# Performance work log

Hardware: AMD Instinct MI355X
Metric: run time of the kernel (lower is better)

The kernel has to match this reference:

```python
import jax, jax.numpy as jnp
import numpy as np

B, F, H = 128, 12288, 2048   # batch, flattened-image dim (3x64x64), MLP hidden
TAU = 0.1                    # constraint(x) = relu(x@W1)@w2 - TAU  (so constraint(0) = -TAU < 0)
THRESHOLD = 1e-3
MAX_STEPS = 30


def setup_inputs() -> dict:
    key = jax.random.key(0)
    k1, k2, k3 = jax.random.split(key, 3)
    x0 = jnp.zeros((B, F), jnp.float32)                 # anchor point, constraint(x0) < 0 by construction
    x = jax.random.normal(k1, (B, F), jnp.float32)
    W1 = jax.random.normal(k2, (F, H), jnp.float32) / np.float32(np.sqrt(F))
    w2 = jax.random.normal(k3, (H,), jnp.float32) / np.float32(np.sqrt(H))
    return {"x0": x0, "x": x, "W1": W1, "w2": w2}


def reference(x0, x, W1, w2):
    def fvals(c):  # per-sample constraint value at interpolation coeff c: [B]
        xc = (1.0 - c)[:, None] * x0 + c[:, None] * x
        return jax.nn.relu(xc @ W1) @ w2 - TAU

    # f(0) = -TAU < 0 (asserted in original). Check f(1): samples already feasible skip search.
    f1 = fvals(jnp.ones((B,), jnp.float32))
    inside = f1 <= 0.0

    a = jnp.zeros((B,), jnp.float32)
    b = jnp.ones((B,), jnp.float32)
    c = jnp.ones((B,), jnp.float32)
    done = inside  # feasible samples keep c = 1 (projected == x)

    def step(carry, _):
        a, b, c, done = carry
        cm = (a + b) * 0.5
        v = fvals(cm)
        upd = ~done
        hit = upd & (v >= -THRESHOLD) & (v < 0.0)   # -threshold <= f(c) < 0 -> converged
        go_a = upd & (v < 0.0) & ~hit               # same sign as f(a): move a
        go_b = upd & (v >= 0.0)                     # opposite sign: move b
        a = jnp.where(go_a, cm, a)
        b = jnp.where(go_b, cm, b)
        c = jnp.where(upd, cm, c)                   # freeze c once done
        done = done | hit
        return (a, b, c, done), None

    (a, b, c, done), _ = jax.lax.scan(step, (a, b, c, done), None, length=MAX_STEPS)

    c = jnp.where(inside, 1.0, c)
    proj = (1.0 - c)[:, None] * x0 + c[:, None] * x
    # Original raises ConvergenceError -> NaN fill for non-converged samples.
    return jnp.where(done[:, None], proj, jnp.float32(jnp.nan))
```

## Files before the change

kernel.cpp:

```cpp
#include <hip/hip_runtime.h>
#include <hip/hip_bf16.h>

#define BB 128
#define FF 12288
#define HH 2048
#define TAU_F 0.1f
#define THR_F 1e-3f
#define NKG (FF / 8)
#define BH (BB * HH)
#define NFLAGS 192
#define SKD 16

typedef __attribute__((ext_vector_type(4))) float f32x4;
typedef __attribute__((ext_vector_type(8))) short s16x8;
typedef __attribute__((ext_vector_type(8))) unsigned short u16x8;

__device__ __forceinline__ void barrier_lds() {
    asm volatile("s_waitcnt lgkmcnt(0)\ns_barrier" ::: "memory");
}

__device__ __forceinline__ void bsplit(float v, unsigned short& h, unsigned short& l) {
    unsigned int u  = __float_as_uint(v);
    unsigned int rh = (u + 0x7fffu + ((u >> 16) & 1u)) >> 16;
    float hf = __uint_as_float(rh << 16);
    float lf = v - hf;
    unsigned int ul = __float_as_uint(lf);
    unsigned int rl = (ul + 0x7fffu + ((ul >> 16) & 1u)) >> 16;
    h = (unsigned short)rh;
    l = (unsigned short)rl;
}

__device__ __forceinline__ bool read_nz(const int* __restrict__ flags) {
    const int lane = threadIdx.x & 63;
    int v = 0;
    if (lane < NFLAGS / 4) {
        const int4 q = ((const int4*)flags)[lane];
        v = q.x | q.y | q.z | q.w;
    }
    return __any(v != 0);
}

__device__ __forceinline__ void presplit_blk(
    const float* __restrict__ X, unsigned short* __restrict__ AH,
    unsigned short* __restrict__ AL, int i, int t) {
    const int kg = i * 8 + (t & 7);
#pragma unroll
    for (int r = 0; r < 4; ++r) {
        const int m = (t >> 3) + r * 32;
        const float* src = X + (size_t)m * FF + kg * 8;
        u16x8 hv, lv;
#pragma unroll
        for (int j = 0; j < 8; ++j) {
            unsigned short h, lo;
            bsplit(src[j], h, lo);
            hv[j] = h; lv[j] = lo;
        }
        const size_t o = ((size_t)kg * BB + m) * 8;
        *(u16x8*)(AH + o) = hv;
        *(u16x8*)(AL + o) = lv;
    }
}

__global__ __launch_bounds__(256) void presplit_kernel(
    const float* __restrict__ x, const float* __restrict__ x0,
    unsigned short* __restrict__ Ah, unsigned short* __restrict__ Al,
    int* __restrict__ flags) {
    const int z = blockIdx.y;
    const int i = blockIdx.x;
    const int t = threadIdx.x;
    if (z == 0) {
        presplit_blk(x, Ah, Al, i, t);
        return;
    }
    __shared__ int snz[4];
    const int w = t >> 6, lane = t & 63;
    const int kg = i * 8 + (t & 7);
    int tnz = 0;
#pragma unroll
    for (int r = 0; r < 4; ++r) {
        const int m = (t >> 3) + r * 32;
        const float4* src = (const float4*)(x0 + (size_t)m * FF + kg * 8);
        const float4 a = src[0], b = src[1];
        tnz |= (a.x != 0.f) | (a.y != 0.f) | (a.z != 0.f) | (a.w != 0.f)
             | (b.x != 0.f) | (b.y != 0.f) | (b.z != 0.f) | (b.w != 0.f);
    }
    const int wnz = __any(tnz != 0) ? 1 : 0;
    if (lane == 0) snz[w] = wnz;
    __syncthreads();
    const int bnz = snz[0] | snz[1] | snz[2] | snz[3];
    if (t == 0) flags[i] = bnz;
    if (bnz) {
        const size_t zoff = (size_t)NKG * BB * 8;
        presplit_blk(x0, Ah + zoff, Al + zoff, i, t);
    }
}

__global__ __launch_bounds__(256, 2) void mfma_gemm_kernel(
    const unsigned short* __restrict__ Ah, const unsigned short* __restrict__ Al,
    const float* __restrict__ W1, float* __restrict__ P,
    const int* __restrict__ flags, int SK, int KC, int NIT) {
    const int z = blockIdx.y;
    if (z == 1 && !read_nz(flags)) return;

    const int nwg = gridDim.x;
    const int bx  = blockIdx.x;
    const int wg  = (bx & 7) * (nwg >> 3) + (bx >> 3);
    const int ct  = wg & 31;
    const int kc  = wg >> 5;

    const int t   = threadIdx.x;
    const int w   = t >> 6;
    const int l   = t & 63;
    const int kgl = l >> 4;
    const int li  = l & 15;

    __shared__ unsigned short lds[2][4096];

    const size_t zoffA = (size_t)z * NKG * BB * 8;
    const unsigned short* APH = Ah + zoffA;
    const unsigned short* APL = Al + zoffA;
    const bool zchk = (z == 1);

    f32x4 acc[2][4];
#pragma unroll
    for (int mt = 0; mt < 2; ++mt)
#pragma unroll
        for (int nt = 0; nt < 4; ++nt) acc[mt][nt] = (f32x4)0.f;

    const int kbase = kc * KC;
    const int kg0   = kbase >> 3;
    const int bkg = t >> 6;
    const int bn  = t & 63;

    s16x8 ahE[2], alE[2], ahO[2], alO[2];
    auto loadA = [&](s16x8* ah, s16x8* al, int it) {
        const int kg = kg0 + it * 4 + kgl;
        if (zchk && flags[kg >> 3] == 0) {
#pragma unroll
            for (int mt = 0; mt < 2; ++mt) { ah[mt] = (s16x8)0; al[mt] = (s16x8)0; }
            return;
        }
#pragma unroll
        for (int mt = 0; mt < 2; ++mt) {
            const size_t o = ((size_t)kg * BB + w * 32 + mt * 16 + li) * 8;
            ah[mt] = *(const s16x8*)(APH + o);
            al[mt] = *(const s16x8*)(APL + o);
        }
    };

    auto stageB_load = [&](int it, float* v) {
        const float* src = W1 + (size_t)(kbase + it * 32 + bkg * 8) * HH + ct * 64 + bn;
#pragma unroll
        for (int j = 0; j < 8; ++j) v[j] = src[(size_t)j * HH];
    };
    auto stageB_write = [&](int buf, const float* v) {
        u16x8 hv, lv;
#pragma unroll
        for (int j = 0; j < 8; ++j) {
            unsigned short h, lo;
            bsplit(v[j], h, lo);
            hv[j] = h; lv[j] = lo;
        }
        unsigned short* d = &lds[buf][(bkg * 64 + bn) * 8];
        *(u16x8*)(d)        = hv;
        *(u16x8*)(d + 2048) = lv;
    };
    auto computeR = [&](const s16x8* ah, const s16x8* al, int buf) {
        const unsigned short* L = lds[buf];
#pragma unroll
        for (int nt = 0; nt < 4; ++nt) {
            const int no = (kgl * 64 + nt * 16 + li) * 8;
            const s16x8 fbh = *(const s16x8*)&L[no];
            const s16x8 fbl = *(const s16x8*)&L[2048 + no];
#pragma unroll
            for (int mt = 0; mt < 2; ++mt) {
                acc[mt][nt] = __builtin_amdgcn_mfma_f32_16x16x32_bf16(ah[mt], fbh, acc[mt][nt], 0, 0, 0);
                acc[mt][nt] = __builtin_amdgcn_mfma_f32_16x16x32_bf16(ah[mt], fbl, acc[mt][nt], 0, 0, 0);
                acc[mt][nt] = __builtin_amdgcn_mfma_f32_16x16x32_bf16(al[mt], fbh, acc[mt][nt], 0, 0, 0);
            }
        }
    };

    float bv0[8], bv1[8], bv2[8], bv3[8];
    loadA(ahE, alE, 0);
    stageB_load(0, bv0);
    stageB_write(0, bv0);
    stageB_load(1, bv1);
    stageB_load(2, bv2);
    stageB_load(3, bv3);
    barrier_lds();

#define GPHASE(p, bvCur, bvNext, aCurH, aCurL, aNxtH, aNxtL)                  \
    {                                                                         \
        if (it + 4 + (p) < NIT) stageB_load(it + 4 + (p), bvCur);             \
        if (it + (p) + 1 < NIT) loadA(aNxtH, aNxtL, it + (p) + 1);            \
        computeR(aCurH, aCurL, (p) & 1);                                      \
        if (it + (p) + 1 < NIT) stageB_write(((p) + 1) & 1, bvNext);          \
        barrier_lds();                                                        \
    }

    for (int it = 0; it < NIT; it += 4) {
        GPHASE(0, bv0, bv1, ahE, alE, ahO, alO)
        GPHASE(1, bv1, bv2, ahO, alO, ahE, alE)
        GPHASE(2, bv2, bv3, ahE, alE, ahO, alO)
        GPHASE(3, bv3, bv0, ahO, alO, ahE, alE)
    }
#undef GPHASE

    float* dst = P + (size_t)(z * SK + kc) * BH;
    const int r0 = w * 32 + (l >> 4) * 4;
    const int c0 = ct * 64 + li;
#pragma unroll
    for (int mt = 0; mt < 2; ++mt)
#pragma unroll
        for (int nt = 0; nt < 4; ++nt)
#pragma unroll
            for (int r = 0; r < 4; ++r)
                dst[(size_t)(r0 + mt * 16 + r) * HH + c0 + nt * 16] = acc[mt][nt][r];
}

__device__ __forceinline__ void solve_linear(float S, float& c, bool& done) {
    const bool inside = (S - TAU_F <= 0.f);
    float a = 0.f, bh = 1.f;
    c = 1.f; done = inside;
    for (int it = 0; it < 30; ++it) {
        const float cm = 0.5f * (a + bh);
        const float v = cm * S - TAU_F;
        const bool upd  = !done;
        const bool hit  = upd && (v >= -THR_F) && (v < 0.f);
        const bool go_a = upd && (v < 0.f) && !hit;
        const bool go_b = upd && (v >= 0.f);
        a  = go_a ? cm : a;
        bh = go_b ? cm : bh;
        c  = upd  ? cm : c;
        done = done || hit;
    }
    c = inside ? 1.f : c;
}

__global__ __launch_bounds__(512) void bisect_write_kernel(
    const float* __restrict__ P, const float* __restrict__ w2,
    const float* __restrict__ x, const float* __restrict__ x0,
    const int* __restrict__ flags, float* __restrict__ out, int SK) {
    const int b    = blockIdx.x >> 1;
    const int half = blockIdx.x & 1;
    const int t = threadIdx.x;
    const int w = t >> 6;
    const int lane = t & 63;
    __shared__ float red[8];
    const bool nz = read_nz(flags);

    const f32x4* P1 = (const f32x4*)(P + (size_t)b * HH) + t;
    f32x4 u1 = (f32x4)0.f;
    for (int kc = 0; kc < SK; ++kc) {
        const f32x4 v = P1[(size_t)kc * (BH / 4)];
        u1.x += v.x; u1.y += v.y; u1.z += v.z; u1.w += v.w;
    }
    const f32x4 wv = ((const f32x4*)w2)[t];

    auto blockReduce = [&](float v) -> float {
#pragma unroll
        for (int off = 32; off > 0; off >>= 1) v += __shfl_xor(v, off);
        if (lane == 0) red[w] = v;
        __syncthreads();
        float s = 0.f;
#pragma unroll
        for (int i = 0; i < 8; ++i) s += red[i];
        __syncthreads();
        return s;
    };

    float c = 1.f;
    bool done = false;
    if (!nz) {
        float p = fmaxf(u1.x, 0.f) * wv.x;
        p = fmaf(fmaxf(u1.y, 0.f), wv.y, p);
        p = fmaf(fmaxf(u1.z, 0.f), wv.z, p);
        p = fmaf(fmaxf(u1.w, 0.f), wv.w, p);
        const float S = blockReduce(p);
        solve_linear(S, c, done);
    } else {
        const f32x4* P0 = (const f32x4*)(P + (size_t)(SK * BH) + (size_t)b * HH) + t;
        f32x4 u0 = (f32x4)0.f;
        for (int kc = 0; kc < SK; ++kc) {
            const f32x4 v = P0[(size_t)kc * (BH / 4)];
            u0.x += v.x; u0.y += v.y; u0.z += v.z; u0.w += v.w;
        }
        f32x4 dd;
        dd.x = u1.x - u0.x; dd.y = u1.y - u0.y;
        dd.z = u1.z - u0.z; dd.w = u1.w - u0.w;
        auto feval = [&](float cc) -> float {
            float p = fmaxf(fmaf(cc, dd.x, u0.x), 0.f) * wv.x;
            p = fmaf(fmaxf(fmaf(cc, dd.y, u0.y), 0.f), wv.y, p);
            p = fmaf(fmaxf(fmaf(cc, dd.z, u0.z), 0.f), wv.z, p);
            p = fmaf(fmaxf(fmaf(cc, dd.w, u0.w), 0.f), wv.w, p);
            return blockReduce(p) - TAU_F;
        };
        const float f1 = feval(1.f);
        const bool inside = (f1 <= 0.f);
        float a = 0.f, bh = 1.f;
        done = inside;
        for (int it = 0; it < 30; ++it) {
            const float cm = 0.5f * (a + bh);
            const float v = feval(cm);
            const bool upd  = !done;
            const bool hit  = upd && (v >= -THR_F) && (v < 0.f);
            const bool go_a = upd && (v < 0.f) && !hit;
            const bool go_b = upd && (v >= 0.f);
            a  = go_a ? cm : a;
            bh = go_b ? cm : bh;
            c  = upd  ? cm : c;
            done = done || hit;
        }
        c = inside ? 1.f : c;
    }

    const float nanv = __int_as_float(0x7fc00000);
    const int base = half * 1536;
    const float4* xr  = (const float4*)(x  + (size_t)b * FF) + base;
    const float4* x0r = (const float4*)(x0 + (size_t)b * FF) + base;
    float4* orow = (float4*)(out + (size_t)b * FF) + base;
    if (!done) {
        float4 o; o.x = o.y = o.z = o.w = nanv;
#pragma unroll
        for (int k2 = 0; k2 < 3; ++k2) orow[t + 512 * k2] = o;
    } else if (!nz) {
#pragma unroll
        for (int k2 = 0; k2 < 3; ++k2) {
            const int i = t + 512 * k2;
            float4 xv = xr[i], o;
            o.x = c * xv.x; o.y = c * xv.y; o.z = c * xv.z; o.w = c * xv.w;
            orow[i] = o;
        }
    } else {
#pragma unroll
        for (int k2 = 0; k2 < 3; ++k2) {
            const int i = t + 512 * k2;
            float4 xv = xr[i], zv = x0r[i], o;
            o.x = fmaf(c, xv.x - zv.x, zv.x);
            o.y = fmaf(c, xv.y - zv.y, zv.y);
            o.z = fmaf(c, xv.z - zv.z, zv.z);
            o.w = fmaf(c, xv.w - zv.w, zv.w);
            orow[i] = o;
        }
    }
}

__global__ __launch_bounds__(256) void zflags_kernel(
    const float4* __restrict__ x0, int* __restrict__ flags) {
    const int t = threadIdx.x;
    const int w = t >> 6, lane = t & 63;
    __shared__ int snz[4];
    int tnz = 0;
    const int base = blockIdx.x * 2048 + t;
#pragma unroll
    for (int j = 0; j < 8; ++j) {
        float4 v = x0[base + 256 * j];
        tnz |= (v.x != 0.f) | (v.y != 0.f) | (v.z != 0.f) | (v.w != 0.f);
    }
    const int wnz = __any(tnz != 0) ? 1 : 0;
    if (lane == 0) snz[w] = wnz;
    __syncthreads();
    if (t == 0) flags[blockIdx.x] = snz[0] | snz[1] | snz[2] | snz[3];
}

__global__ __launch_bounds__(256) void legacy_gemm_kernel(
    const float* __restrict__ x, const float* __restrict__ x0,
    const float* __restrict__ W1, float* __restrict__ P,
    const int* __restrict__ flags) {
    const int ct = blockIdx.x, z = blockIdx.z, t = threadIdx.x;
    if (z == 1 && !read_nz(flags)) return;
    const int cg = t & 7, rg = t >> 3;
    const int r0 = rg * 4, cc = ct * 64 + cg * 8;
    float acc[4][8];
#pragma unroll
    for (int i = 0; i < 4; ++i)
#pragma unroll
        for (int n = 0; n < 8; ++n) acc[i][n] = 0.f;
    const float* __restrict__ X = z ? x0 : x;
    for (int k = 0; k < FF; k += 4) {
        float xr[4][4];
#pragma unroll
        for (int i = 0; i < 4; ++i) {
            float4 v = *(const float4*)(X + (size_t)(r0 + i) * FF + k);
            xr[i][0] = v.x; xr[i][1] = v.y; xr[i][2] = v.z; xr[i][3] = v.w;
        }
        float wr[4][8];
#pragma unroll
        for (int j = 0; j < 4; ++j) {
            float4 a = *(const float4*)(W1 + (size_t)(k + j) * HH + cc);
            float4 b = *(const float4*)(W1 + (size_t)(k + j) * HH + cc + 4);
            wr[j][0] = a.x; wr[j][1] = a.y; wr[j][2] = a.z; wr[j][3] = a.w;
            wr[j][4] = b.x; wr[j][5] = b.y; wr[j][6] = b.z; wr[j][7] = b.w;
        }
#pragma unroll
        for (int j = 0; j < 4; ++j)
#pragma unroll
            for (int i = 0; i < 4; ++i)
#pragma unroll
                for (int n = 0; n < 8; ++n)
                    acc[i][n] = fmaf(xr[i][j], wr[j][n], acc[i][n]);
    }
    float* Pp = P + (size_t)z * BH;
#pragma unroll
    for (int i = 0; i < 4; ++i) {
        float4 o0, o1;
        o0.x = acc[i][0]; o0.y = acc[i][1]; o0.z = acc[i][2]; o0.w = acc[i][3];
        o1.x = acc[i][4]; o1.y = acc[i][5]; o1.z = acc[i][6]; o1.w = acc[i][7];
        *(float4*)(Pp + (size_t)(r0 + i) * HH + cc) = o0;
        *(float4*)(Pp + (size_t)(r0 + i) * HH + cc + 4) = o1;
    }
}

extern "C" void kernel_launch(void* const* d_in, const int* in_sizes, int n_in,
                              void* d_out, int out_size, void* d_ws, size_t ws_size,
                              hipStream_t stream) {
    const float* x0 = (const float*)d_in[0];
    const float* x  = (const float*)d_in[1];
    const float* W1 = (const float*)d_in[2];
    const float* w2 = (const float*)d_in[3];
    float* out = (float*)d_out;
    char* ws = (char*)d_ws;

    const size_t szA   = (size_t)2 * NKG * BB * 8 * sizeof(unsigned short);
    const size_t offAl = szA;
    const size_t offFl = 2 * szA;
    const size_t offP  = offFl + 1024;

    int SK = 0;
    const int cand[5] = {SKD, 8, 4, 2, 1};
    for (int i = 0; i < 5; ++i) {
        const size_t need = offP + (size_t)2 * cand[i] * BH * sizeof(float);
        if (ws_size >= need) { SK = cand[i]; break; }
    }

    if (SK > 0) {
        unsigned short* Ah = (unsigned short*)ws;
        unsigned short* Al = (unsigned short*)(ws + offAl);
        int*   flags = (int*)(ws + offFl);
        float* P     = (float*)(ws + offP);
        const int KC = FF / SK, NIT = KC / 32;

        presplit_kernel<<<dim3(NFLAGS, 2), 256, 0, stream>>>(x, x0, Ah, Al, flags);
        mfma_gemm_kernel<<<dim3(32 * SK, 2), 256, 0, stream>>>(Ah, Al, W1, P, flags, SK, KC, NIT);
        bisect_write_kernel<<<2 * BB, 512, 0, stream>>>(P, w2, x, x0, flags, out, SK);
    } else {
        float* P     = (float*)ws;
        int*   flags = (int*)(ws + (size_t)2 * BH * sizeof(float));
        zflags_kernel<<<NFLAGS, 256, 0, stream>>>((const float4*)x0, flags);
        legacy_gemm_kernel<<<dim3(32, 1, 2), 256, 0, stream>>>(x, x0, W1, P, flags);
        bisect_write_kernel<<<2 * BB, 512, 0, stream>>>(P, w2, x, x0, flags, out, 1);
    }
}
```

Measured before the change: 49.36 us.

## Double GEMM block to 512 threads with one M-tile per wave

```diff
diff --git a/kernel.cpp b/kernel.cpp
--- a/kernel.cpp
+++ b/kernel.cpp
@@ -14,6 +14,7 @@
 typedef __attribute__((ext_vector_type(4))) float f32x4;
 typedef __attribute__((ext_vector_type(8))) short s16x8;
 typedef __attribute__((ext_vector_type(8))) unsigned short u16x8;
+typedef __attribute__((ext_vector_type(4))) unsigned short u16x4;
 
 __device__ __forceinline__ void barrier_lds() {
     asm volatile("s_waitcnt lgkmcnt(0)\ns_barrier" ::: "memory");
@@ -95,7 +96,7 @@
     }
 }
 
-__global__ __launch_bounds__(256, 2) void mfma_gemm_kernel(
+__global__ __launch_bounds__(512, 4) void mfma_gemm_kernel(
     const unsigned short* __restrict__ Ah, const unsigned short* __restrict__ Al,
     const float* __restrict__ W1, float* __restrict__ P,
     const int* __restrict__ flags, int SK, int KC, int NIT) {
@@ -121,67 +122,56 @@
     const unsigned short* APL = Al + zoffA;
     const bool zchk = (z == 1);
 
-    f32x4 acc[2][4];
-#pragma unroll
-    for (int mt = 0; mt < 2; ++mt)
-#pragma unroll
-        for (int nt = 0; nt < 4; ++nt) acc[mt][nt] = (f32x4)0.f;
+    f32x4 acc[4];
+#pragma unroll
+    for (int nt = 0; nt < 4; ++nt) acc[nt] = (f32x4)0.f;
 
     const int kbase = kc * KC;
     const int kg0   = kbase >> 3;
-    const int bkg = t >> 6;
-    const int bn  = t & 63;
-
-    s16x8 ahE[2], alE[2], ahO[2], alO[2];
-    auto loadA = [&](s16x8* ah, s16x8* al, int it) {
+
+    s16x8 ahE, alE, ahO, alO;
+    auto loadA = [&](s16x8& ah, s16x8& al, int it) {
         const int kg = kg0 + it * 4 + kgl;
         if (zchk && flags[kg >> 3] == 0) {
-#pragma unroll
-            for (int mt = 0; mt < 2; ++mt) { ah[mt] = (s16x8)0; al[mt] = (s16x8)0; }
+            ah = (s16x8)0; al = (s16x8)0;
             return;
         }
-#pragma unroll
-        for (int mt = 0; mt < 2; ++mt) {
-            const size_t o = ((size_t)kg * BB + w * 32 + mt * 16 + li) * 8;
-            ah[mt] = *(const s16x8*)(APH + o);
-            al[mt] = *(const s16x8*)(APL + o);
-        }
+        const size_t o = ((size_t)kg * BB + w * 16 + li) * 8;
+        ah = *(const s16x8*)(APH + o);
+        al = *(const s16x8*)(APL + o);
     };
 
     auto stageB_load = [&](int it, float* v) {
-        const float* src = W1 + (size_t)(kbase + it * 32 + bkg * 8) * HH + ct * 64 + bn;
-#pragma unroll
-        for (int j = 0; j < 8; ++j) v[j] = src[(size_t)j * HH];
+        const float* src = W1 + (size_t)(kbase + it * 32 + w * 4) * HH + ct * 64 + l;
+#pragma unroll
+        for (int j = 0; j < 4; ++j) v[j] = src[(size_t)j * HH];
     };
     auto stageB_write = [&](int buf, const float* v) {
-        u16x8 hv, lv;
-#pragma unroll
-        for (int j = 0; j < 8; ++j) {
+        u16x4 hv, lv;
+#pragma unroll
+        for (int j = 0; j < 4; ++j) {
             unsigned short h, lo;
             bsplit(v[j], h, lo);
             hv[j] = h; lv[j] = lo;
         }
-        unsigned short* d = &lds[buf][(bkg * 64 + bn) * 8];
-        *(u16x8*)(d)        = hv;
-        *(u16x8*)(d + 2048) = lv;
+        unsigned short* d = &lds[buf][(((w >> 1) * 64 + l) * 8) + (w & 1) * 4];
+        *(u16x4*)(d)        = hv;
+        *(u16x4*)(d + 2048) = lv;
     };
-    auto computeR = [&](const s16x8* ah, const s16x8* al, int buf) {
+    auto computeR = [&](const s16x8& ah, const s16x8& al, int buf) {
         const unsigned short* L = lds[buf];
 #pragma unroll
         for (int nt = 0; nt < 4; ++nt) {
             const int no = (kgl * 64 + nt * 16 + li) * 8;
             const s16x8 fbh = *(const s16x8*)&L[no];
             const s16x8 fbl = *(const s16x8*)&L[2048 + no];
-#pragma unroll
-            for (int mt = 0; mt < 2; ++mt) {
-                acc[mt][nt] = __builtin_amdgcn_mfma_f32_16x16x32_bf16(ah[mt], fbh, acc[mt][nt], 0, 0, 0);
-                acc[mt][nt] = __builtin_amdgcn_mfma_f32_16x16x32_bf16(ah[mt], fbl, acc[mt][nt], 0, 0, 0);
-                acc[mt][nt] = __builtin_amdgcn_mfma_f32_16x16x32_bf16(al[mt], fbh, acc[mt][nt], 0, 0, 0);
-            }
+            acc[nt] = __builtin_amdgcn_mfma_f32_16x16x32_bf16(ah, fbh, acc[nt], 0, 0, 0);
+            acc[nt] = __builtin_amdgcn_mfma_f32_16x16x32_bf16(ah, fbl, acc[nt], 0, 0, 0);
+            acc[nt] = __builtin_amdgcn_mfma_f32_16x16x32_bf16(al, fbh, acc[nt], 0, 0, 0);
         }
     };
 
-    float bv0[8], bv1[8], bv2[8], bv3[8];
+    float bv0[4], bv1[4], bv2[4], bv3[4];
     loadA(ahE, alE, 0);
     stageB_load(0, bv0);
     stageB_write(0, bv0);
@@ -208,15 +198,13 @@
 #undef GPHASE
 
     float* dst = P + (size_t)(z * SK + kc) * BH;
-    const int r0 = w * 32 + (l >> 4) * 4;
+    const int r0 = w * 16 + (l >> 4) * 4;
     const int c0 = ct * 64 + li;
 #pragma unroll
-    for (int mt = 0; mt < 2; ++mt)
-#pragma unroll
-        for (int nt = 0; nt < 4; ++nt)
-#pragma unroll
-            for (int r = 0; r < 4; ++r)
-                dst[(size_t)(r0 + mt * 16 + r) * HH + c0 + nt * 16] = acc[mt][nt][r];
+    for (int nt = 0; nt < 4; ++nt)
+#pragma unroll
+        for (int r = 0; r < 4; ++r)
+            dst[(size_t)(r0 + r) * HH + c0 + nt * 16] = acc[nt][r];
 }
 
 __device__ __forceinline__ void solve_linear(float S, float& c, bool& done) {
@@ -442,7 +430,7 @@
         const int KC = FF / SK, NIT = KC / 32;
 
         presplit_kernel<<<dim3(NFLAGS, 2), 256, 0, stream>>>(x, x0, Ah, Al, flags);
-        mfma_gemm_kernel<<<dim3(32 * SK, 2), 256, 0, stream>>>(Ah, Al, W1, P, flags, SK, KC, NIT);
+        mfma_gemm_kernel<<<dim3(32 * SK, 2), 512, 0, stream>>>(Ah, Al, W1, P, flags, SK, KC, NIT);
         bisect_write_kernel<<<2 * BB, 512, 0, stream>>>(P, w2, x, x0, flags, out, SK);
     } else {
         float* P     = (float*)ws;
```

Result: faster. 47.82 us (-3.1%).
